# Performance work log

Hardware: AMD Instinct MI355X
Metric: run time of the kernel (lower is better)

Reference implementation:

```python
import jax, jax.numpy as jnp
import numpy as np

N, E, DIM = 20000, 500000, 2
KS = 5                 # kernel size per pseudo-dim (open spline)
K = KS ** DIM          # 25 kernel weight matrices (+1 root weight)
IN_F, OUT_F = 64, 64
S = 2 ** DIM           # support size of degree-1 B-spline basis


def setup_inputs() -> dict:
    key = jax.random.key(0)
    k1, k2, k3, k4, k5 = jax.random.split(key, 5)
    x = jax.random.normal(k1, (N, IN_F), jnp.float32)
    edge_index = jax.random.randint(k2, (2, E), 0, N)          # row=target, col=source
    pseudo = jax.random.uniform(k3, (E, DIM), jnp.float32)     # u(i,j) in [0,1]^dim
    weight = jax.random.normal(k4, (K + 1, IN_F, OUT_F), jnp.float32) * 0.05
    bias = jax.random.normal(k5, (OUT_F,), jnp.float32) * 0.05
    return {"x": x, "edge_index": edge_index, "pseudo": pseudo,
            "weight": weight, "bias": bias}


def _spline_basis(pseudo):
    """Degree-1 open B-spline tensor-product basis.
    Returns basis values [E,S] and flat kernel indices [E,S]."""
    u = pseudo * (KS - 1)                                      # [E,DIM]
    i0 = jnp.clip(jnp.floor(u).astype(jnp.int32), 0, KS - 2)   # lower knot per dim
    frac = u - i0.astype(u.dtype)                              # [E,DIM]
    bases, idxs = [], []
    for s in range(S):
        b = jnp.ones((pseudo.shape[0],), pseudo.dtype)
        idx = jnp.zeros((pseudo.shape[0],), jnp.int32)
        for d in range(DIM):
            bit = (s >> d) & 1
            w = frac[:, d] if bit else (1.0 - frac[:, d])
            b = b * w
            idx = idx * KS + (i0[:, d] + bit)                  # row-major flat index
        bases.append(b)
        idxs.append(idx)
    return jnp.stack(bases, 1), jnp.stack(idxs, 1)             # [E,S], [E,S]


def reference(x, edge_index, pseudo, weight, bias):
    row, col = edge_index[0], edge_index[1]
    basis, kidx = _spline_basis(pseudo)                        # [E,S]
    xj = x[col]                                                # gather neighbors [E,IN]
    # scatter B-spline-weighted neighbor features into (target node, kernel idx) buckets
    seg = (row[:, None].astype(jnp.int32) * K + kidx).reshape(-1)          # [E*S]
    vals = (basis[:, :, None] * xj[:, None, :]).reshape(-1, IN_F)          # [E*S,IN]
    agg = jax.ops.segment_sum(vals, seg, num_segments=N * K)
    agg = agg.reshape(N, K, IN_F)
    out = jnp.einsum('nki,kio->no', agg, weight[:K])           # basis-indexed matmuls
    deg = jax.ops.segment_sum(jnp.ones((E,), x.dtype), row, num_segments=N)
    out = out / jnp.clip(deg, 1.0)[:, None]                    # 1/|N(i)| normalization
    out = out + x @ weight[K] + bias                           # root weight + bias
    return out
```

## Files before the change

### kernel.cpp

```cpp
#include <hip/hip_runtime.h>
#include <hip/hip_bf16.h>
#include <cstdint>

constexpr int N_NODES = 20000;
constexpr int N_EDGES = 500000;
constexpr int IN_F    = 64;
constexpr int OUT_F   = 64;
constexpr int KS      = 5;
constexpr int K_MATS  = 25;
constexpr int NK      = 26;
constexpr int ZSTRIDE = NK * OUT_F;

typedef __attribute__((ext_vector_type(8))) short short8;
typedef __attribute__((ext_vector_type(4))) float f32x4;

__device__ __forceinline__ ushort f2bf(float f) {
    union { float f; uint32_t u; } c; c.f = f;
    uint32_t u = c.u + 0x7FFFu + ((c.u >> 16) & 1u);
    return (ushort)(u >> 16);
}
__device__ __forceinline__ float bf2f(ushort s) {
    union { uint32_t u; float f; } c; c.u = ((uint32_t)s) << 16;
    return c.f;
}


__global__ void k_hist(const int* __restrict__ ei, int* __restrict__ cnt) {
    int e = blockIdx.x * blockDim.x + threadIdx.x;
    if (e < N_EDGES) atomicAdd(&cnt[ei[e]], 1);
}

__global__ __launch_bounds__(1024) void k_scan(const int* __restrict__ cnt,
                                               int* __restrict__ row_start) {
    __shared__ int sums[1024];
    const int T = 1024;
    int tid = threadIdx.x;
    const int per = (N_NODES + T - 1) / T;
    int base = tid * per;
    int s = 0;
    for (int j = 0; j < per; ++j) {
        int idx = base + j;
        if (idx < N_NODES) s += cnt[idx];
    }
    sums[tid] = s;
    __syncthreads();
    for (int off = 1; off < T; off <<= 1) {
        int v = (tid >= off) ? sums[tid - off] : 0;
        __syncthreads();
        sums[tid] += v;
        __syncthreads();
    }
    int run = (tid == 0) ? 0 : sums[tid - 1];
    for (int j = 0; j < per; ++j) {
        int idx = base + j;
        if (idx < N_NODES) { row_start[idx] = run; run += cnt[idx]; }
    }
    if (tid == T - 1) row_start[N_NODES] = run;
}

__global__ void k_fill(const int* __restrict__ ei, const float* __restrict__ pseudo,
                       const int* __restrict__ row_start, int* __restrict__ fill_pos,
                       int* __restrict__ col_sorted, int* __restrict__ kpack_sorted,
                       float4* __restrict__ basis_sorted) {
    int e = blockIdx.x * blockDim.x + threadIdx.x;
    if (e >= N_EDGES) return;
    int row = ei[e];
    int col = ei[N_EDGES + e];
    float u0 = pseudo[2 * e]     * (float)(KS - 1);
    float u1 = pseudo[2 * e + 1] * (float)(KS - 1);
    int i0 = min(max((int)floorf(u0), 0), KS - 2);
    int i1 = min(max((int)floorf(u1), 0), KS - 2);
    float f0 = u0 - (float)i0;
    float f1 = u1 - (float)i1;
    float b00 = (1.f - f0) * (1.f - f1);
    float b10 = f0 * (1.f - f1);
    float b01 = (1.f - f0) * f1;
    float b11 = f0 * f1;
    int k00 = i0 * KS + i1;
    int k10 = (i0 + 1) * KS + i1;
    int k01 = i0 * KS + (i1 + 1);
    int k11 = (i0 + 1) * KS + (i1 + 1);
    int pos = row_start[row] + atomicAdd(&fill_pos[row], 1);
    col_sorted[pos] = col;
    kpack_sorted[pos] = k00 | (k10 << 8) | (k01 << 16) | (k11 << 24);
    basis_sorted[pos] = make_float4(b00, b10, b01, b11);
}

__global__ void k_prep(const float* __restrict__ w, ushort* __restrict__ wb) {
    int t = blockIdx.x * blockDim.x + threadIdx.x;
    if (t >= NK * 2 * 4 * 64) return;
    int lane = t & 63;
    int nf   = (t >> 6) & 3;
    int ks   = (t >> 8) & 1;
    int k    = t >> 9;
    int kk0  = ks * 32 + (lane >> 4) * 8;
    int col  = nf * 16 + (lane & 15);
    ushort v[8];
#pragma unroll
    for (int j = 0; j < 8; ++j)
        v[j] = f2bf(w[(k * 64 + kk0 + j) * 64 + col]);
    uint4 p;
    p.x = (uint32_t)v[0] | ((uint32_t)v[1] << 16);
    p.y = (uint32_t)v[2] | ((uint32_t)v[3] << 16);
    p.z = (uint32_t)v[4] | ((uint32_t)v[5] << 16);
    p.w = (uint32_t)v[6] | ((uint32_t)v[7] << 16);
    ((uint4*)wb)[t] = p;
}

__global__ __launch_bounds__(256) void k_z(const float* __restrict__ x,
                                           const ushort* __restrict__ wb,
                                           ushort* __restrict__ z) {
    int lane = threadIdx.x & 63;
    int wave = threadIdx.x >> 6;
    int node0 = blockIdx.x * 16;
    int r  = lane & 15;
    int kg = lane >> 4;

    short8 a[2];
#pragma unroll
    for (int ks = 0; ks < 2; ++ks) {
        const float4* xp = (const float4*)(x + (node0 + r) * IN_F + ks * 32 + kg * 8);
        float4 x0 = xp[0];
        float4 x1 = xp[1];
        short8 af;
        af[0] = (short)f2bf(x0.x); af[1] = (short)f2bf(x0.y);
        af[2] = (short)f2bf(x0.z); af[3] = (short)f2bf(x0.w);
        af[4] = (short)f2bf(x1.x); af[5] = (short)f2bf(x1.y);
        af[6] = (short)f2bf(x1.z); af[7] = (short)f2bf(x1.w);
        a[ks] = af;
    }

    for (int k = wave; k < NK; k += 4) {
        f32x4 acc[4];
#pragma unroll
        for (int nf = 0; nf < 4; ++nf) acc[nf] = (f32x4){0.f, 0.f, 0.f, 0.f};

#pragma unroll
        for (int ks = 0; ks < 2; ++ks) {
#pragma unroll
            for (int nf = 0; nf < 4; ++nf) {
                union { uint4 u; short8 s; } b;
                b.u = *(const uint4*)(wb + ((((size_t)k * 2 + ks) * 4 + nf) * 64 + lane) * 8);
                acc[nf] = __builtin_amdgcn_mfma_f32_16x16x32_bf16(a[ks], b.s, acc[nf], 0, 0, 0);
            }
        }
        int rowbase = (lane >> 4) * 4;
#pragma unroll
        for (int nf = 0; nf < 4; ++nf) {
#pragma unroll
            for (int rg = 0; rg < 4; ++rg) {
                int row = rowbase + rg;
                z[(size_t)(node0 + row) * ZSTRIDE + k * 64 + nf * 16 + (lane & 15)] =
                    f2bf(acc[nf][rg]);
            }
        }
    }
}

__global__ __launch_bounds__(256) void k_out(const ushort* __restrict__ z,
        const float* __restrict__ bias, const int* __restrict__ row_start,
        const int* __restrict__ col_sorted, const int* __restrict__ kpack,
        const float4* __restrict__ basis4, float* __restrict__ out) {
    int lane = threadIdx.x & 63;
    int n = blockIdx.x * 4 + (threadIdx.x >> 6);
    if (n >= N_NODES) return;
    int e0 = row_start[n], e1 = row_start[n + 1];
    float acc = 0.f;
    for (int e = e0; e < e1; ++e) {
        int col = col_sorted[e];
        int kp  = kpack[e];
        float4 b = basis4[e];
        const ushort* zb = z + (size_t)col * ZSTRIDE;
        float z0 = bf2f(zb[((kp      ) & 255) * 64 + lane]);
        float z1 = bf2f(zb[((kp >> 8 ) & 255) * 64 + lane]);
        float z2 = bf2f(zb[((kp >> 16) & 255) * 64 + lane]);
        float z3 = bf2f(zb[((kp >> 24) & 255) * 64 + lane]);
        acc += b.x * z0 + b.y * z1 + b.z * z2 + b.w * z3;
    }
    int deg = e1 - e0;
    float root = bf2f(z[(size_t)n * ZSTRIDE + K_MATS * 64 + lane]);
    out[n * OUT_F + lane] = acc / (float)max(deg, 1) + root + bias[lane];
}


extern "C" void kernel_launch(void* const* d_in, const int* in_sizes, int n_in,
                              void* d_out, int out_size, void* d_ws, size_t ws_size,
                              hipStream_t stream) {
    const float* x      = (const float*)d_in[0];
    const int*   ei     = (const int*)d_in[1];
    const float* pseudo = (const float*)d_in[2];
    const float* weight = (const float*)d_in[3];
    const float* bias   = (const float*)d_in[4];
    float* out = (float*)d_out;

    char* ws = (char*)d_ws;
    int* cnt       = (int*)(ws + 0);
    int* fill_pos  = (int*)(ws + 80000);
    int* row_start = (int*)(ws + 160000);
    int* col_sorted   = (int*)(ws + 240128);
    int* kpack_sorted = (int*)(ws + 2240128);
    float4* basis_sorted = (float4*)(ws + 4240128);
    ushort* wb = (ushort*)(ws + 12240128);
    ushort* zb = (ushort*)(ws + 12453120);

    hipMemsetAsync(ws, 0, 160000, stream);

    int eb = (N_EDGES + 255) / 256;
    k_hist<<<eb, 256, 0, stream>>>(ei, cnt);
    k_scan<<<1, 1024, 0, stream>>>(cnt, row_start);
    k_fill<<<eb, 256, 0, stream>>>(ei, pseudo, row_start, fill_pos,
                                   col_sorted, kpack_sorted, basis_sorted);
    k_prep<<<(NK * 2 * 4 * 64 + 255) / 256, 256, 0, stream>>>(weight, wb);
    k_z<<<N_NODES / 16, 256, 0, stream>>>(x, wb, zb);
    k_out<<<(N_NODES + 3) / 4, 256, 0, stream>>>(zb, bias, row_start,
                                                 col_sorted, kpack_sorted,
                                                 basis_sorted, out);
}
```

Before: 237.8 us.

## Pack edge records, tile z layout, fuse prep/hist, unroll gather loop

Merges weight prep and histogram into one launch, packs col/kernel-index/bf16 basis into a single 16-byte sorted edge record, and re-tiles z so each (node-tile, kernel) slab is contiguous, staging MFMA output through LDS for vectorized 16-byte stores. The aggregation kernel batches eight edge records at a time with two accumulators to raise memory-level parallelism in the gather. Basis weights are now stored in bf16, which cuts record traffic but adds rounding error.

```diff
diff --git a/kernel.cpp b/kernel.cpp
--- a/kernel.cpp
+++ b/kernel.cpp
@@ -9,7 +9,7 @@
 constexpr int KS      = 5;
 constexpr int K_MATS  = 25;
 constexpr int NK      = 26;
-constexpr int ZSTRIDE = NK * OUT_F;
+constexpr int ZTILE_USH = 1024;
 
 typedef __attribute__((ext_vector_type(8))) short short8;
 typedef __attribute__((ext_vector_type(4))) float f32x4;
@@ -19,15 +19,39 @@
     uint32_t u = c.u + 0x7FFFu + ((c.u >> 16) & 1u);
     return (ushort)(u >> 16);
 }
-__device__ __forceinline__ float bf2f(ushort s) {
-    union { uint32_t u; float f; } c; c.u = ((uint32_t)s) << 16;
+__device__ __forceinline__ float bf2f(uint32_t s) {
+    union { uint32_t u; float f; } c; c.u = (s & 0xFFFFu) << 16;
     return c.f;
 }
 
-
-__global__ void k_hist(const int* __restrict__ ei, int* __restrict__ cnt) {
-    int e = blockIdx.x * blockDim.x + threadIdx.x;
-    if (e < N_EDGES) atomicAdd(&cnt[ei[e]], 1);
+constexpr int PREP_BLOCKS = (NK * 2 * 4 * 64) / 256;
+constexpr int HIST_BLOCKS = (N_EDGES + 255) / 256;
+
+__global__ void k_ph(const float* __restrict__ w, ushort* __restrict__ wb,
+                     const int* __restrict__ ei, int* __restrict__ cnt) {
+    int b = blockIdx.x;
+    if (b < PREP_BLOCKS) {
+        int t = b * 256 + threadIdx.x;
+        int lane = t & 63;
+        int nf   = (t >> 6) & 3;
+        int ks   = (t >> 8) & 1;
+        int k    = t >> 9;
+        int kk0  = ks * 32 + (lane >> 4) * 8;
+        int col  = nf * 16 + (lane & 15);
+        ushort v[8];
+#pragma unroll
+        for (int j = 0; j < 8; ++j)
+            v[j] = f2bf(w[(k * 64 + kk0 + j) * 64 + col]);
+        uint4 p;
+        p.x = (uint32_t)v[0] | ((uint32_t)v[1] << 16);
+        p.y = (uint32_t)v[2] | ((uint32_t)v[3] << 16);
+        p.z = (uint32_t)v[4] | ((uint32_t)v[5] << 16);
+        p.w = (uint32_t)v[6] | ((uint32_t)v[7] << 16);
+        ((uint4*)wb)[t] = p;
+    } else {
+        int e = (b - PREP_BLOCKS) * 256 + threadIdx.x;
+        if (e < N_EDGES) atomicAdd(&cnt[ei[e]], 1);
+    }
 }
 
 __global__ __launch_bounds__(1024) void k_scan(const int* __restrict__ cnt,
@@ -60,8 +84,7 @@
 
 __global__ void k_fill(const int* __restrict__ ei, const float* __restrict__ pseudo,
                        const int* __restrict__ row_start, int* __restrict__ fill_pos,
-                       int* __restrict__ col_sorted, int* __restrict__ kpack_sorted,
-                       float4* __restrict__ basis_sorted) {
+                       uint4* __restrict__ rec) {
     int e = blockIdx.x * blockDim.x + threadIdx.x;
     if (e >= N_EDGES) return;
     int row = ei[e];
@@ -78,41 +101,25 @@
     float b11 = f0 * f1;
     int k00 = i0 * KS + i1;
     int k10 = (i0 + 1) * KS + i1;
-    int k01 = i0 * KS + (i1 + 1);
-    int k11 = (i0 + 1) * KS + (i1 + 1);
+    int k01 = k00 + 1;
+    int k11 = k10 + 1;
     int pos = row_start[row] + atomicAdd(&fill_pos[row], 1);
-    col_sorted[pos] = col;
-    kpack_sorted[pos] = k00 | (k10 << 8) | (k01 << 16) | (k11 << 24);
-    basis_sorted[pos] = make_float4(b00, b10, b01, b11);
-}
-
-__global__ void k_prep(const float* __restrict__ w, ushort* __restrict__ wb) {
-    int t = blockIdx.x * blockDim.x + threadIdx.x;
-    if (t >= NK * 2 * 4 * 64) return;
-    int lane = t & 63;
-    int nf   = (t >> 6) & 3;
-    int ks   = (t >> 8) & 1;
-    int k    = t >> 9;
-    int kk0  = ks * 32 + (lane >> 4) * 8;
-    int col  = nf * 16 + (lane & 15);
-    ushort v[8];
-#pragma unroll
-    for (int j = 0; j < 8; ++j)
-        v[j] = f2bf(w[(k * 64 + kk0 + j) * 64 + col]);
-    uint4 p;
-    p.x = (uint32_t)v[0] | ((uint32_t)v[1] << 16);
-    p.y = (uint32_t)v[2] | ((uint32_t)v[3] << 16);
-    p.z = (uint32_t)v[4] | ((uint32_t)v[5] << 16);
-    p.w = (uint32_t)v[6] | ((uint32_t)v[7] << 16);
-    ((uint4*)wb)[t] = p;
+    uint4 r;
+    r.x = (uint32_t)col;
+    r.y = (uint32_t)(k00 | (k10 << 8) | (k01 << 16) | (k11 << 24));
+    r.z = (uint32_t)f2bf(b00) | ((uint32_t)f2bf(b10) << 16);
+    r.w = (uint32_t)f2bf(b01) | ((uint32_t)f2bf(b11) << 16);
+    rec[pos] = r;
 }
 
 __global__ __launch_bounds__(256) void k_z(const float* __restrict__ x,
                                            const ushort* __restrict__ wb,
                                            ushort* __restrict__ z) {
+    __shared__ float lds[4][16][66];
     int lane = threadIdx.x & 63;
     int wave = threadIdx.x >> 6;
-    int node0 = blockIdx.x * 16;
+    int tile = blockIdx.x;
+    int node0 = tile * 16;
     int r  = lane & 15;
     int kg = lane >> 4;
 
@@ -144,42 +151,99 @@
                 acc[nf] = __builtin_amdgcn_mfma_f32_16x16x32_bf16(a[ks], b.s, acc[nf], 0, 0, 0);
             }
         }
-        int rowbase = (lane >> 4) * 4;
-#pragma unroll
-        for (int nf = 0; nf < 4; ++nf) {
-#pragma unroll
-            for (int rg = 0; rg < 4; ++rg) {
-                int row = rowbase + rg;
-                z[(size_t)(node0 + row) * ZSTRIDE + k * 64 + nf * 16 + (lane & 15)] =
-                    f2bf(acc[nf][rg]);
-            }
-        }
+#pragma unroll
+        for (int nf = 0; nf < 4; ++nf)
+#pragma unroll
+            for (int rg = 0; rg < 4; ++rg)
+                lds[wave][kg * 4 + rg][nf * 16 + r] = acc[nf][rg];
+        asm volatile("s_waitcnt lgkmcnt(0)" ::: "memory");
+        __builtin_amdgcn_sched_barrier(0);
+        const float* lrow = &lds[wave][lane >> 2][(lane & 3) * 16];
+        float v[16];
+#pragma unroll
+        for (int j = 0; j < 16; ++j) v[j] = lrow[j];
+        uint32_t pk[8];
+#pragma unroll
+        for (int j = 0; j < 8; ++j)
+            pk[j] = (uint32_t)f2bf(v[2 * j]) | ((uint32_t)f2bf(v[2 * j + 1]) << 16);
+        uint4* dst = (uint4*)(z + (size_t)(tile * NK + k) * ZTILE_USH + lane * 16);
+        dst[0] = make_uint4(pk[0], pk[1], pk[2], pk[3]);
+        dst[1] = make_uint4(pk[4], pk[5], pk[6], pk[7]);
+        asm volatile("" ::: "memory");
     }
 }
 
 __global__ __launch_bounds__(256) void k_out(const ushort* __restrict__ z,
         const float* __restrict__ bias, const int* __restrict__ row_start,
-        const int* __restrict__ col_sorted, const int* __restrict__ kpack,
-        const float4* __restrict__ basis4, float* __restrict__ out) {
+        const uint4* __restrict__ rec, float* __restrict__ out) {
     int lane = threadIdx.x & 63;
     int n = blockIdx.x * 4 + (threadIdx.x >> 6);
     if (n >= N_NODES) return;
     int e0 = row_start[n], e1 = row_start[n + 1];
-    float acc = 0.f;
-    for (int e = e0; e < e1; ++e) {
-        int col = col_sorted[e];
-        int kp  = kpack[e];
-        float4 b = basis4[e];
-        const ushort* zb = z + (size_t)col * ZSTRIDE;
-        float z0 = bf2f(zb[((kp      ) & 255) * 64 + lane]);
-        float z1 = bf2f(zb[((kp >> 8 ) & 255) * 64 + lane]);
-        float z2 = bf2f(zb[((kp >> 16) & 255) * 64 + lane]);
-        float z3 = bf2f(zb[((kp >> 24) & 255) * 64 + lane]);
-        acc += b.x * z0 + b.y * z1 + b.z * z2 + b.w * z3;
+    float acc0 = 0.f, acc1 = 0.f;
+    int e = e0;
+    for (; e + 8 <= e1; e += 8) {
+        uint4 rr[8];
+#pragma unroll
+        for (int t = 0; t < 8; ++t) rr[t] = rec[e + t];
+        float vv[8][4];
+#pragma unroll
+        for (int t = 0; t < 8; ++t) {
+            uint32_t kp = rr[t].y;
+            const ushort* zb = z + (size_t)(rr[t].x >> 4) * (NK * ZTILE_USH)
+                                 + (rr[t].x & 15) * 64 + lane;
+            vv[t][0] = bf2f((uint32_t)zb[((kp      ) & 255) * ZTILE_USH]);
+            vv[t][1] = bf2f((uint32_t)zb[((kp >> 8 ) & 255) * ZTILE_USH]);
+            vv[t][2] = bf2f((uint32_t)zb[((kp >> 16) & 255) * ZTILE_USH]);
+            vv[t][3] = bf2f((uint32_t)zb[((kp >> 24)      ) * ZTILE_USH]);
+        }
+#pragma unroll
+        for (int t = 0; t < 8; ++t) {
+            float b0 = bf2f(rr[t].z), b1 = bf2f(rr[t].z >> 16);
+            float b2 = bf2f(rr[t].w), b3 = bf2f(rr[t].w >> 16);
+            float s = b0 * vv[t][0] + b1 * vv[t][1] + b2 * vv[t][2] + b3 * vv[t][3];
+            if (t & 1) acc1 += s; else acc0 += s;
+        }
+    }
+    for (; e + 4 <= e1; e += 4) {
+        uint4 rr[4];
+#pragma unroll
+        for (int t = 0; t < 4; ++t) rr[t] = rec[e + t];
+        float vv[4][4];
+#pragma unroll
+        for (int t = 0; t < 4; ++t) {
+            uint32_t kp = rr[t].y;
+            const ushort* zb = z + (size_t)(rr[t].x >> 4) * (NK * ZTILE_USH)
+                                 + (rr[t].x & 15) * 64 + lane;
+            vv[t][0] = bf2f((uint32_t)zb[((kp      ) & 255) * ZTILE_USH]);
+            vv[t][1] = bf2f((uint32_t)zb[((kp >> 8 ) & 255) * ZTILE_USH]);
+            vv[t][2] = bf2f((uint32_t)zb[((kp >> 16) & 255) * ZTILE_USH]);
+            vv[t][3] = bf2f((uint32_t)zb[((kp >> 24)      ) * ZTILE_USH]);
+        }
+#pragma unroll
+        for (int t = 0; t < 4; ++t) {
+            float b0 = bf2f(rr[t].z), b1 = bf2f(rr[t].z >> 16);
+            float b2 = bf2f(rr[t].w), b3 = bf2f(rr[t].w >> 16);
+            float s = b0 * vv[t][0] + b1 * vv[t][1] + b2 * vv[t][2] + b3 * vv[t][3];
+            if (t & 1) acc1 += s; else acc0 += s;
+        }
+    }
+    for (; e < e1; ++e) {
+        uint4 r = rec[e];
+        uint32_t kp = r.y;
+        const ushort* zb = z + (size_t)(r.x >> 4) * (NK * ZTILE_USH)
+                             + (r.x & 15) * 64 + lane;
+        float v0 = bf2f((uint32_t)zb[((kp      ) & 255) * ZTILE_USH]);
+        float v1 = bf2f((uint32_t)zb[((kp >> 8 ) & 255) * ZTILE_USH]);
+        float v2 = bf2f((uint32_t)zb[((kp >> 16) & 255) * ZTILE_USH]);
+        float v3 = bf2f((uint32_t)zb[((kp >> 24)      ) * ZTILE_USH]);
+        acc0 += bf2f(r.z) * v0 + bf2f(r.z >> 16) * v1
+              + bf2f(r.w) * v2 + bf2f(r.w >> 16) * v3;
     }
     int deg = e1 - e0;
-    float root = bf2f(z[(size_t)n * ZSTRIDE + K_MATS * 64 + lane]);
-    out[n * OUT_F + lane] = acc / (float)max(deg, 1) + root + bias[lane];
+    float root = bf2f((uint32_t)z[(size_t)((n >> 4) * NK + K_MATS) * ZTILE_USH
+                                  + (n & 15) * 64 + lane]);
+    out[n * OUT_F + lane] = (acc0 + acc1) / (float)max(deg, 1) + root + bias[lane];
 }
 
 
@@ -197,22 +261,15 @@
     int* cnt       = (int*)(ws + 0);
     int* fill_pos  = (int*)(ws + 80000);
     int* row_start = (int*)(ws + 160000);
-    int* col_sorted   = (int*)(ws + 240128);
-    int* kpack_sorted = (int*)(ws + 2240128);
-    float4* basis_sorted = (float4*)(ws + 4240128);
-    ushort* wb = (ushort*)(ws + 12240128);
-    ushort* zb = (ushort*)(ws + 12453120);
+    uint4* rec     = (uint4*)(ws + 240128);
+    ushort* wb     = (ushort*)(ws + 8240128);
+    ushort* zb     = (ushort*)(ws + 8453120);
 
     hipMemsetAsync(ws, 0, 160000, stream);
 
-    int eb = (N_EDGES + 255) / 256;
-    k_hist<<<eb, 256, 0, stream>>>(ei, cnt);
+    k_ph<<<PREP_BLOCKS + HIST_BLOCKS, 256, 0, stream>>>(weight, wb, ei, cnt);
     k_scan<<<1, 1024, 0, stream>>>(cnt, row_start);
-    k_fill<<<eb, 256, 0, stream>>>(ei, pseudo, row_start, fill_pos,
-                                   col_sorted, kpack_sorted, basis_sorted);
-    k_prep<<<(NK * 2 * 4 * 64 + 255) / 256, 256, 0, stream>>>(weight, wb);
+    k_fill<<<HIST_BLOCKS, 256, 0, stream>>>(ei, pseudo, row_start, fill_pos, rec);
     k_z<<<N_NODES / 16, 256, 0, stream>>>(x, wb, zb);
-    k_out<<<(N_NODES + 3) / 4, 256, 0, stream>>>(zb, bias, row_start,
-                                                 col_sorted, kpack_sorted,
-                                                 basis_sorted, out);
-}
+    k_out<<<(N_NODES + 3) / 4, 256, 0, stream>>>(zb, bias, row_start, rec, out);
+}
```

Result: faster. 209.7 us (-11.8%).
